# Performance work log

Measured on AMD Instinct MI355X. Metric: run time of the kernel, lower is better.

Reference implementation:

```python
import jax, jax.numpy as jnp
import numpy as np

D_MODEL = 1024
NUM_HEADS = 16
KERNEL_EPS = 1e-4
NORM_STAB = 1e-6


def setup_inputs() -> dict:
    key = jax.random.key(0)
    k1, k2, k3, k4 = jax.random.split(key, 4)
    B, L = 4, 2048
    d_head, m = D_MODEL // NUM_HEADS, 256
    return {
        "query": jax.random.normal(k1, (B, L, D_MODEL), jnp.float32),
        "key": jax.random.normal(k2, (B, L, D_MODEL), jnp.float32),
        "value": jax.random.normal(k3, (B, L, D_MODEL), jnp.float32),
        # random projection matrix (fixed, not learned); original uses orthogonal blocks
        "random_features": jax.random.normal(k4, (d_head, m), jnp.float32),
    }


def _performer_forward(query, key, value, random_features):
    B, L, dm = query.shape
    h = NUM_HEADS
    d = dm // h
    m = random_features.shape[1]

    def split_heads(x):  # [B,L,dm] -> [B,h,L,d]
        return x.reshape(B, L, h, d).transpose(0, 2, 1, 3)

    q, k, v = split_heads(query), split_heads(key), split_heads(value)

    # FAVOR+ exp kernel with stabilizers (matches get_projected_queries_and_keys)
    scale = dm ** -0.25
    q = q * scale
    k = k * scale
    proj_q = jnp.einsum('bhld,dm->bhlm', q, random_features)
    proj_k = jnp.einsum('bhld,dm->bhlm', k, random_features)
    h_q = -0.5 * jnp.sum(q * q, axis=-1, keepdims=True)  # [B,h,L,1]
    h_k = -0.5 * jnp.sum(k * k, axis=-1, keepdims=True)
    q_stab = h_q  # reduce_max over a keepdims size-1 axis == identity (faithful)
    k_stab = jnp.max(h_k)  # global scalar
    q_kernel = jnp.exp(h_q + (proj_q - q_stab))
    k_kernel = jnp.exp(h_k + (proj_k - k_stab))
    nc = m ** -0.5
    q_prime = nc * (q_kernel + KERNEL_EPS)  # [B,h,L,m]
    k_prime = nc * (k_kernel + KERNEL_EPS)

    # Causal linear attention: streaming prefix state instead of [B,h,L,m,d] cumsum
    qp = q_prime.transpose(2, 0, 1, 3)  # [L,B,h,m]
    kp = k_prime.transpose(2, 0, 1, 3)
    vp = v.transpose(2, 0, 1, 3)        # [L,B,h,d]

    def step(carry, inp):
        S, Z = carry                      # S:[B,h,m,d], Z:[B,h,m]
        qt, kt, vt = inp
        S = S + kt[..., :, None] * vt[..., None, :]
        Z = Z + kt
        num = jnp.einsum('bhm,bhmd->bhd', qt, S)
        den = jnp.einsum('bhm,bhm->bh', qt, Z)
        return (S, Z), (num, den)

    S0 = jnp.zeros((B, h, m, d), q_prime.dtype)
    Z0 = jnp.zeros((B, h, m), q_prime.dtype)
    _, (nums, dens) = jax.lax.scan(step, (S0, Z0), (qp, kp, vp))
    nums = nums.transpose(1, 2, 0, 3)          # [B,h,L,d]
    dens = dens.transpose(1, 2, 0)[..., None]  # [B,h,L,1]

    # stabilize denominator near zero (matches _denominator_...)
    extreme = (jnp.abs(dens) <= NORM_STAB).astype(dens.dtype)
    dens = dens + 2.0 * NORM_STAB * extreme
    out = nums / dens

    # merge heads -> [B,L,dm]
    return out.transpose(0, 2, 1, 3).reshape(B, L, dm)


def reference(query, key, value, random_features):
    return _performer_forward(query, key, value, random_features)
```

## Files before the change

### kernel.cpp

```cpp
#include <hip/hip_runtime.h>


#define BB 4
#define HH 16
#define LL 2048
#define DH 64
#define DM 1024
#define MM 256
#define CC 64
#define NCH (LL / CC)

constexpr float SCALE = 0.17677669529663687f;
constexpr float NCF   = 0.0625f;
constexpr float LNCF  = -2.772588722239781f;
constexpr float KEPS  = 1e-4f;
constexpr float NCFK  = NCF * KEPS;
constexpr float NSTB  = 1e-6f;

typedef __attribute__((ext_vector_type(8))) short s16x8;
typedef __attribute__((ext_vector_type(4))) float f32x4;

__device__ __forceinline__ float bf2f(unsigned short s) {
  return __uint_as_float(((unsigned)s) << 16);
}
__device__ __forceinline__ unsigned short f2bf(float f) {
  return __builtin_bit_cast(unsigned short, static_cast<__bf16>(f));
}
__device__ __forceinline__ unsigned enc_key(float f) {
  unsigned u = __float_as_uint(f);
  return (u & 0x80000000u) ? ~u : (u | 0x80000000u);
}
__device__ __forceinline__ float dec_key(unsigned k) {
  unsigned u = (k & 0x80000000u) ? (k & 0x7FFFFFFFu) : ~k;
  return __uint_as_float(u);
}

__global__ __launch_bounds__(256) void kstab_kernel(const float* __restrict__ Kin,
                                                    unsigned int* __restrict__ wsu) {
  int lane = threadIdx.x & 63;
  int wave = threadIdx.x >> 6;
  int base = blockIdx.x * 64 + wave * 16;
  float m = -3.4e38f;
  for (int it = 0; it < 16; ++it) {
    int r = base + it;
    float v = Kin[(size_t)r * 64 + lane];
    float s = v * v;
    #pragma unroll
    for (int off = 32; off; off >>= 1) s += __shfl_xor(s, off, 64);
    float hk = -0.5f * (SCALE * SCALE) * s;
    m = fmaxf(m, hk);
  }
  __shared__ float wmax[4];
  if (lane == 0) wmax[wave] = m;
  __syncthreads();
  if (threadIdx.x == 0) {
    float mm = fmaxf(fmaxf(wmax[0], wmax[1]), fmaxf(wmax[2], wmax[3]));
    atomicMax(wsu, enc_key(mm));
  }
}

__global__ __launch_bounds__(256) void rft_prep(const float* __restrict__ RF,
                                                unsigned short* __restrict__ RFTg) {
  int m = threadIdx.x;
  float rv[64];
  #pragma unroll
  for (int d = 0; d < 64; ++d) rv[d] = RF[d * MM + m];
  unsigned swz = (unsigned)((m & 7) << 4);
  #pragma unroll
  for (int c16 = 0; c16 < 8; ++c16) {
    union { unsigned short u[8]; uint4 v; } pk_;
    #pragma unroll
    for (int i = 0; i < 8; ++i) pk_.u[i] = f2bf(rv[c16 * 8 + i]);
    unsigned byte = (unsigned)(m * 128) + (((unsigned)(c16 * 16)) ^ swz);
    *(uint4*)((char*)RFTg + byte) = pk_.v;
  }
}

__global__ __launch_bounds__(256) void phase1_kernel(const float* __restrict__ Kin,
                                                     const float* __restrict__ Vin,
                                                     const unsigned short* __restrict__ RFTg,
                                                     unsigned short* __restrict__ wsSb,
                                                     float* __restrict__ wsZ,
                                                     const unsigned int* __restrict__ wsu,
                                                     int bh0) {
  __shared__ __align__(16) char lds[45056];
  char* U0  = lds;
  char* KPl = lds + 16384;
  char* VT  = lds + 32768;
  float* Zw = (float*)(lds + 40960);

  int slice = blockIdx.x / NCH;
  int c     = blockIdx.x % NCH;
  int bh = bh0 + slice, b = bh >> 4, h = bh & 15;
  const int t    = threadIdx.x;
  const int lane = t & 63;
  const int w    = t >> 6;
  const int rloc = lane & 15;
  const int kc0  = (lane >> 4) * 8;
  const int arow = 16 * w + rloc;
  const unsigned lgrp16 = (unsigned)((lane >> 4) * 16);
  float kst = dec_key(*wsu);

  const float* krow = Kin + ((size_t)(b * LL + c * CC + arow)) * DM + h * DH;
  s16x8 kfrag[2];
  float ss = 0.f;
  #pragma unroll
  for (int kf = 0; kf < 2; ++kf) {
    float4 ka_ = *(const float4*)(krow + kf * 32 + kc0);
    float4 kb_ = *(const float4*)(krow + kf * 32 + kc0 + 4);
    float ks[8] = {ka_.x, ka_.y, ka_.z, ka_.w, kb_.x, kb_.y, kb_.z, kb_.w};
    #pragma unroll
    for (int i = 0; i < 8; ++i) {
      float kv = ks[i] * SCALE;
      ss += kv * kv;
      kfrag[kf][i] = (short)f2bf(kv);
    }
  }
  ss += __shfl_xor(ss, 16, 64);
  ss += __shfl_xor(ss, 32, 64);
  float hkv = -0.5f * ss;
  float hkb[4];
  #pragma unroll
  for (int r = 0; r < 4; ++r)
    hkb[r] = __shfl(hkv, (lane >> 4) * 4 + r, 64) - kst + LNCF;

  {
    const float* vbase = Vin + ((size_t)(b * LL + c * CC + w * 16)) * DM + h * DH + lane;
    float vv[16];
    #pragma unroll
    for (int i = 0; i < 16; ++i) vv[i] = vbase[(size_t)i * DM];
    unsigned swz = (unsigned)((lane & 7) << 4);
    #pragma unroll
    for (int q = 0; q < 2; ++q) {
      union { unsigned short u[8]; uint4 v; } pk_;
      #pragma unroll
      for (int i = 0; i < 8; ++i) pk_.u[i] = f2bf(vv[q * 8 + i]);
      unsigned byte = (unsigned)(lane * 128) + (((unsigned)(w * 32 + q * 16)) ^ swz);
      *(uint4*)(VT + byte) = pk_.v;
    }
  }

  for (int h2 = 0; h2 < 2; ++h2) {
    __syncthreads();
    {
      const uint4* src = (const uint4*)(RFTg + (size_t)h2 * 8192);
      uint4* dst = (uint4*)U0;
      #pragma unroll
      for (int r2 = 0; r2 < 4; ++r2) dst[t + 256 * r2] = src[t + 256 * r2];
    }
    __syncthreads();

    f32x4 pk[8];
    #pragma unroll
    for (int i = 0; i < 8; ++i) pk[i] = (f32x4)0.f;
    #pragma unroll
    for (int mt = 0; mt < 8; ++mt) {
      int mloc = mt * 16 + rloc;
      unsigned rbyte = (unsigned)(mloc * 128);
      unsigned swz = (unsigned)((mloc & 7) << 4);
      #pragma unroll
      for (int kf = 0; kf < 2; ++kf) {
        s16x8 bf_ = *(const s16x8*)(U0 + rbyte + (((unsigned)(kf * 64) + lgrp16) ^ swz));
        pk[mt] = __builtin_amdgcn_mfma_f32_16x16x32_bf16(kfrag[kf], bf_, pk[mt], 0, 0, 0);
      }
    }
    #pragma unroll
    for (int mt = 0; mt < 8; ++mt) {
      int mloc = mt * 16 + rloc;
      float zp = 0.f;
      #pragma unroll
      for (int r = 0; r < 4; ++r) {
        int cpos = 16 * w + (lane >> 4) * 4 + r;
        float kpv = __expf(hkb[r] + pk[mt][r]) + NCFK;
        zp += kpv;
        unsigned byte = (unsigned)(mloc * 128) +
                        (((unsigned)(cpos * 2)) ^ ((unsigned)((mloc & 7) << 4)));
        *(unsigned short*)(KPl + byte) = f2bf(kpv);
      }
      zp += __shfl_xor(zp, 16, 64);
      zp += __shfl_xor(zp, 32, 64);
      if (lane < 16) Zw[w * 256 + h2 * 128 + mt * 16 + lane] = zp;
    }
    __syncthreads();

    f32x4 sacc[8];
    #pragma unroll
    for (int i = 0; i < 8; ++i) sacc[i] = (f32x4)0.f;
    s16x8 af[2];
    {
      int drow = w * 16 + rloc;
      unsigned rbyte = (unsigned)(drow * 128);
      unsigned swz = (unsigned)((drow & 7) << 4);
      #pragma unroll
      for (int kf = 0; kf < 2; ++kf)
        af[kf] = *(const s16x8*)(VT + rbyte + (((unsigned)(kf * 64) + lgrp16) ^ swz));
    }
    #pragma unroll
    for (int mt = 0; mt < 8; ++mt) {
      int mrow = mt * 16 + rloc;
      unsigned rbyte = (unsigned)(mrow * 128);
      unsigned swz = (unsigned)((mrow & 7) << 4);
      #pragma unroll
      for (int kf = 0; kf < 2; ++kf) {
        s16x8 bf_ = *(const s16x8*)(KPl + rbyte + (((unsigned)(kf * 64) + lgrp16) ^ swz));
        sacc[mt] = __builtin_amdgcn_mfma_f32_16x16x32_bf16(af[kf], bf_, sacc[mt], 0, 0, 0);
      }
    }
    unsigned short* sdst = wsSb + (size_t)(slice * NCH + c) * 16384;
    #pragma unroll
    for (int mt = 0; mt < 8; ++mt) {
      #pragma unroll
      for (int r = 0; r < 4; ++r) {
        int d = w * 16 + (lane >> 4) * 4 + r;
        int m = h2 * 128 + mt * 16 + rloc;
        sdst[d * 256 + m] = f2bf(sacc[mt][r]);
      }
    }
  }
  __syncthreads();
  float z = Zw[t] + Zw[256 + t] + Zw[512 + t] + Zw[768 + t];
  wsZ[(size_t)(slice * NCH + c) * MM + t] = z;
}

__global__ __launch_bounds__(256) void scan_kernel(const unsigned short* __restrict__ wsSb,
                                                   unsigned short* __restrict__ wsPb,
                                                   float* __restrict__ wsZ) {
  int slice = blockIdx.x >> 3, part = blockIdx.x & 7;
  const int t = threadIdx.x;
  int d_l = t >> 5, moct = t & 31;
  int d = part * 8 + d_l, m0 = moct * 8;
  int half = m0 >> 7, m_l = m0 & 127;
  const unsigned short* srcb = wsSb + (size_t)slice * NCH * 16384 + d * 256 + m0;
  char* dstb = (char*)wsPb + ((size_t)slice * NCH * 2 + half) * 16384 +
               (unsigned)(d * 256) + (((unsigned)(m_l * 2)) ^ ((unsigned)((d & 7) << 4)));
  float run[8] = {0.f, 0.f, 0.f, 0.f, 0.f, 0.f, 0.f, 0.f};
  for (int c = 0; c < NCH; ++c) {
    uint4 v = *(const uint4*)(srcb + (size_t)c * 16384);
    union { unsigned short u[8]; uint4 q; } o;
    #pragma unroll
    for (int i = 0; i < 8; ++i) o.u[i] = f2bf(run[i]);
    *(uint4*)(dstb + (size_t)c * 32768) = o.q;
    const unsigned short* pv = (const unsigned short*)&v;
    #pragma unroll
    for (int i = 0; i < 8; ++i) run[i] += bf2f(pv[i]);
  }
  if (part == 0) {
    for (int e = t; e < MM; e += 256) {
      float zr = 0.f;
      for (int c = 0; c < NCH; ++c) {
        size_t idx = (size_t)slice * NCH * MM + (size_t)c * MM + e;
        float x = wsZ[idx];
        wsZ[idx] = zr;
        zr += x;
      }
    }
  }
}

__global__ __launch_bounds__(256) void phase3_kernel(const float* __restrict__ Qin,
                                                     const float* __restrict__ Kin,
                                                     const float* __restrict__ Vin,
                                                     const unsigned short* __restrict__ RFTg,
                                                     const unsigned short* __restrict__ wsPb,
                                                     const float* __restrict__ wsZ,
                                                     const unsigned int* __restrict__ wsu,
                                                     float* __restrict__ Out,
                                                     int bh0) {
  __shared__ __align__(16) char lds[50176];
  char* U0  = lds;
  char* QPl = lds + 16384;
  char* KPl = lds + 32768;
  float* ZL = (float*)(lds + 49152);

  int slice = blockIdx.x / NCH;
  int c     = blockIdx.x % NCH;
  int bh = bh0 + slice, b = bh >> 4, h = bh & 15;
  const int t    = threadIdx.x;
  const int lane = t & 63;
  const int w    = t >> 6;

  ZL[t] = wsZ[(size_t)(slice * NCH + c) * MM + t];
  float kst = dec_key(*wsu);

  const int rloc = lane & 15;
  const int kc0  = (lane >> 4) * 8;
  const int arow = 16 * w + rloc;
  const float* qrow = Qin + ((size_t)(b * LL + c * CC + arow)) * DM + h * DH;
  const float* krow = Kin + ((size_t)(b * LL + c * CC + arow)) * DM + h * DH;

  s16x8 qfrag[2], kfrag[2];
  float ss = 0.f;
  #pragma unroll
  for (int kf = 0; kf < 2; ++kf) {
    float4 qa_ = *(const float4*)(qrow + kf * 32 + kc0);
    float4 qb_ = *(const float4*)(qrow + kf * 32 + kc0 + 4);
    float4 ka_ = *(const float4*)(krow + kf * 32 + kc0);
    float4 kb_ = *(const float4*)(krow + kf * 32 + kc0 + 4);
    float qs[8] = {qa_.x, qa_.y, qa_.z, qa_.w, qb_.x, qb_.y, qb_.z, qb_.w};
    float ks[8] = {ka_.x, ka_.y, ka_.z, ka_.w, kb_.x, kb_.y, kb_.z, kb_.w};
    #pragma unroll
    for (int i = 0; i < 8; ++i) {
      float qv = qs[i] * SCALE, kv = ks[i] * SCALE;
      ss += kv * kv;
      qfrag[kf][i] = (short)f2bf(qv);
      kfrag[kf][i] = (short)f2bf(kv);
    }
  }
  ss += __shfl_xor(ss, 16, 64);
  ss += __shfl_xor(ss, 32, 64);
  float hkv = -0.5f * ss;

  f32x4 Aacc[4], Oacc[4];
  #pragma unroll
  for (int i = 0; i < 4; ++i) { Aacc[i] = (f32x4)0.f; Oacc[i] = (f32x4)0.f; }
  float den1[4] = {0.f, 0.f, 0.f, 0.f};
  float den2[4] = {0.f, 0.f, 0.f, 0.f};

  float hkb[4];
  #pragma unroll
  for (int r = 0; r < 4; ++r)
    hkb[r] = __shfl(hkv, (lane >> 4) * 4 + r, 64) - kst + LNCF;

  const unsigned lgrp16 = (unsigned)((lane >> 4) * 16);

  for (int h2 = 0; h2 < 2; ++h2) {
    __syncthreads();
    {
      const uint4* src = (const uint4*)(RFTg + (size_t)h2 * 8192);
      uint4* dst = (uint4*)U0;
      #pragma unroll
      for (int r2 = 0; r2 < 4; ++r2) dst[t + 256 * r2] = src[t + 256 * r2];
    }
    __syncthreads();

    f32x4 pq[8], pk[8];
    #pragma unroll
    for (int i = 0; i < 8; ++i) { pq[i] = (f32x4)0.f; pk[i] = (f32x4)0.f; }
    #pragma unroll
    for (int mt = 0; mt < 8; ++mt) {
      int mloc = mt * 16 + rloc;
      unsigned rbyte = (unsigned)(mloc * 128);
      unsigned swz = (unsigned)((mloc & 7) << 4);
      #pragma unroll
      for (int kf = 0; kf < 2; ++kf) {
        s16x8 bf_ = *(const s16x8*)(U0 + rbyte + (((unsigned)(kf * 64) + lgrp16) ^ swz));
        pq[mt] = __builtin_amdgcn_mfma_f32_16x16x32_bf16(qfrag[kf], bf_, pq[mt], 0, 0, 0);
        pk[mt] = __builtin_amdgcn_mfma_f32_16x16x32_bf16(kfrag[kf], bf_, pk[mt], 0, 0, 0);
      }
    }
    #pragma unroll
    for (int mt = 0; mt < 8; ++mt) {
      int mloc = mt * 16 + rloc;
      #pragma unroll
      for (int r = 0; r < 4; ++r) {
        int row = 16 * w + (lane >> 4) * 4 + r;
        float qpv = __expf(pq[mt][r] + LNCF) + NCFK;
        float kpv = __expf(hkb[r] + pk[mt][r]) + NCFK;
        unsigned byte = (unsigned)(row * 256) +
                        (((unsigned)(mloc * 2)) ^ ((unsigned)((row & 7) << 4)));
        *(unsigned short*)(QPl + byte) = f2bf(qpv);
        *(unsigned short*)(KPl + byte) = f2bf(kpv);
        den2[r] += qpv * ZL[h2 * 128 + mloc];
      }
    }
    __syncthreads();

    uint4 stmp[4];
    {
      const char* ssrc = (const char*)wsPb + ((size_t)(slice * NCH + c) * 2 + h2) * 16384;
      #pragma unroll
      for (int r2 = 0; r2 < 4; ++r2)
        stmp[r2] = *(const uint4*)(ssrc + t * 16 + r2 * 4096);
    }

    s16x8 qa[4];
    {
      unsigned rbyte = (unsigned)(arow * 256);
      unsigned swz = (unsigned)((arow & 7) << 4);
      #pragma unroll
      for (int kf = 0; kf < 4; ++kf)
        qa[kf] = *(const s16x8*)(QPl + rbyte + (((unsigned)(kf * 64) + lgrp16) ^ swz));
    }
    for (int ct = 0; ct <= w; ++ct) {
      int rowb = ct * 16 + rloc;
      unsigned rbyte = (unsigned)(rowb * 256);
      unsigned swz = (unsigned)((rowb & 7) << 4);
      #pragma unroll
      for (int kf = 0; kf < 4; ++kf) {
        s16x8 bf_ = *(const s16x8*)(KPl + rbyte + (((unsigned)(kf * 64) + lgrp16) ^ swz));
        Aacc[ct] = __builtin_amdgcn_mfma_f32_16x16x32_bf16(qa[kf], bf_, Aacc[ct], 0, 0, 0);
      }
    }
    {
      uint4* u0v = (uint4*)U0;
      #pragma unroll
      for (int r2 = 0; r2 < 4; ++r2) u0v[t + 256 * r2] = stmp[r2];
    }
    __syncthreads();

    #pragma unroll
    for (int ct = 0; ct < 4; ++ct) {
      int rowb = ct * 16 + rloc;
      unsigned rbyte = (unsigned)(rowb * 256);
      unsigned swz = (unsigned)((rowb & 7) << 4);
      #pragma unroll
      for (int kf = 0; kf < 4; ++kf) {
        s16x8 bf_ = *(const s16x8*)(U0 + rbyte + (((unsigned)(kf * 64) + lgrp16) ^ swz));
        Oacc[ct] = __builtin_amdgcn_mfma_f32_16x16x32_bf16(qa[kf], bf_, Oacc[ct], 0, 0, 0);
      }
    }
  }

  __syncthreads();

  #pragma unroll
  for (int ct = 0; ct < 4; ++ct) {
    #pragma unroll
    for (int r = 0; r < 4; ++r) {
      int row = 16 * w + (lane >> 4) * 4 + r;
      int col = ct * 16 + rloc;
      float av = (ct <= w && col <= row) ? Aacc[ct][r] : 0.f;
      den1[r] += av;
      unsigned byte = (unsigned)(row * 128) +
                      (((unsigned)(col * 2)) ^ ((unsigned)((row & 7) << 4)));
      *(unsigned short*)(U0 + byte) = f2bf(av);
    }
  }
  {
    const float* vbase = Vin + ((size_t)(b * LL + c * CC + w * 16)) * DM + h * DH + lane;
    float vv[16];
    #pragma unroll
    for (int i = 0; i < 16; ++i) vv[i] = vbase[(size_t)i * DM];
    unsigned swz = (unsigned)((lane & 7) << 4);
    #pragma unroll
    for (int q = 0; q < 2; ++q) {
      union { unsigned short u[8]; uint4 v; } pk_;
      #pragma unroll
      for (int i = 0; i < 8; ++i) pk_.u[i] = f2bf(vv[q * 8 + i]);
      unsigned byte = 8192u + (unsigned)(lane * 128) + (((unsigned)(w * 32 + q * 16)) ^ swz);
      *(uint4*)(U0 + byte) = pk_.v;
    }
  }
  __syncthreads();

  {
    int nkf = (w >= 2) ? 2 : 1;
    unsigned arbyte = (unsigned)(arow * 128);
    unsigned aswz = (unsigned)((arow & 7) << 4);
    for (int kf = 0; kf < nkf; ++kf) {
      s16x8 af = *(const s16x8*)(U0 + arbyte + (((unsigned)(kf * 64) + lgrp16) ^ aswz));
      #pragma unroll
      for (int ct = 0; ct < 4; ++ct) {
        int rowv = ct * 16 + rloc;
        unsigned byte = 8192u + (unsigned)(rowv * 128) +
                        (((unsigned)(kf * 64) + lgrp16) ^ ((unsigned)((rowv & 7) << 4)));
        s16x8 vf = *(const s16x8*)(U0 + byte);
        Oacc[ct] = __builtin_amdgcn_mfma_f32_16x16x32_bf16(af, vf, Oacc[ct], 0, 0, 0);
      }
    }
  }

  float inv[4];
  #pragma unroll
  for (int r = 0; r < 4; ++r) {
    float dv = den1[r] + den2[r];
    dv += __shfl_xor(dv, 1, 64);
    dv += __shfl_xor(dv, 2, 64);
    dv += __shfl_xor(dv, 4, 64);
    dv += __shfl_xor(dv, 8, 64);
    if (fabsf(dv) <= NSTB) dv += 2.f * NSTB;
    inv[r] = 1.0f / dv;
  }
  #pragma unroll
  for (int r = 0; r < 4; ++r) {
    int row = 16 * w + (lane >> 4) * 4 + r;
    size_t g = ((size_t)(b * LL + c * CC + row)) * DM + h * DH;
    #pragma unroll
    for (int ct = 0; ct < 4; ++ct) {
      Out[g + ct * 16 + rloc] = Oacc[ct][r] * inv[r];
    }
  }
}

extern "C" void kernel_launch(void* const* d_in, const int* in_sizes, int n_in,
                              void* d_out, int out_size, void* d_ws, size_t ws_size,
                              hipStream_t stream) {
  const float* Q  = (const float*)d_in[0];
  const float* K  = (const float*)d_in[1];
  const float* V  = (const float*)d_in[2];
  const float* RF = (const float*)d_in[3];
  float* Out = (float*)d_out;
  unsigned int* wsu = (unsigned int*)d_ws;

  const size_t RESV = 1024;
  const size_t RFTB = 32768;
  const size_t perSlice = (size_t)NCH * 16384 * 2
                        + (size_t)NCH * 2 * 16384
                        + (size_t)NCH * MM * 4;
  int G = BB * HH;
  while (G > 1 && RESV + RFTB + (size_t)G * perSlice > ws_size) G >>= 1;

  unsigned short* RFTg = (unsigned short*)((char*)d_ws + RESV);
  unsigned short* wsSb = (unsigned short*)((char*)d_ws + RESV + RFTB);
  unsigned short* wsPb = wsSb + (size_t)G * NCH * 16384;
  float* wsZ = (float*)((char*)wsPb + (size_t)G * NCH * 2 * 16384);

  hipMemsetAsync(d_ws, 0, 4, stream);
  hipLaunchKernelGGL(kstab_kernel, dim3(2048), dim3(256), 0, stream, K, wsu);
  hipLaunchKernelGGL(rft_prep, dim3(1), dim3(256), 0, stream, RF, RFTg);
  for (int bh0 = 0; bh0 < BB * HH; bh0 += G) {
    hipLaunchKernelGGL(phase1_kernel, dim3(G * NCH), dim3(256), 0, stream,
                       K, V, RFTg, wsSb, wsZ, wsu, bh0);
    hipLaunchKernelGGL(scan_kernel, dim3(G * 8), dim3(256), 0, stream, wsSb, wsPb, wsZ);
    hipLaunchKernelGGL(phase3_kernel, dim3(G * NCH), dim3(256), 0, stream,
                       Q, K, V, RFTg, wsPb, wsZ, wsu, Out, bh0);
  }
}
```

Baseline: 160.9 us.

## Repartition phase1 projection by m-columns per wave and overwrite RF buffer in place

Each wave now loads all 64 key rows of the chunk as MFMA fragments and computes the projection for its own 32 random-feature columns, instead of 16 rows against all 128 columns. The exp'd kernel values are written back into the same LDS rows that held the random features, which removes the separate K' buffer and the four-way Z partial reduction. This cuts the LDS footprint from about 44KB to 25KB, which may allow more resident blocks. The cost is four times the key fragment registers per thread and some extra shuffles for the row norms.

```diff
diff --git a/kernel.cpp b/kernel.cpp
--- a/kernel.cpp
+++ b/kernel.cpp
@@ -83,11 +83,10 @@
                                                      float* __restrict__ wsZ,
                                                      const unsigned int* __restrict__ wsu,
                                                      int bh0) {
-  __shared__ __align__(16) char lds[45056];
-  char* U0  = lds;
-  char* KPl = lds + 16384;
-  char* VT  = lds + 32768;
-  float* Zw = (float*)(lds + 40960);
+  __shared__ __align__(16) char lds[25600];
+  char* B0  = lds;
+  char* VT  = lds + 16384;
+  float* Zw = (float*)(lds + 24576);
 
   int slice = blockIdx.x / NCH;
   int c     = blockIdx.x % NCH;
@@ -97,32 +96,31 @@
   const int w    = t >> 6;
   const int rloc = lane & 15;
   const int kc0  = (lane >> 4) * 8;
-  const int arow = 16 * w + rloc;
   const unsigned lgrp16 = (unsigned)((lane >> 4) * 16);
   float kst = dec_key(*wsu);
 
-  const float* krow = Kin + ((size_t)(b * LL + c * CC + arow)) * DM + h * DH;
-  s16x8 kfrag[2];
-  float ss = 0.f;
-  #pragma unroll
-  for (int kf = 0; kf < 2; ++kf) {
-    float4 ka_ = *(const float4*)(krow + kf * 32 + kc0);
-    float4 kb_ = *(const float4*)(krow + kf * 32 + kc0 + 4);
-    float ks[8] = {ka_.x, ka_.y, ka_.z, ka_.w, kb_.x, kb_.y, kb_.z, kb_.w};
-    #pragma unroll
-    for (int i = 0; i < 8; ++i) {
-      float kv = ks[i] * SCALE;
-      ss += kv * kv;
-      kfrag[kf][i] = (short)f2bf(kv);
-    }
-  }
-  ss += __shfl_xor(ss, 16, 64);
-  ss += __shfl_xor(ss, 32, 64);
-  float hkv = -0.5f * ss;
-  float hkb[4];
-  #pragma unroll
-  for (int r = 0; r < 4; ++r)
-    hkb[r] = __shfl(hkv, (lane >> 4) * 4 + r, 64) - kst + LNCF;
+  s16x8 kfrag[4][2];
+  float hkv[4];
+  #pragma unroll
+  for (int rb = 0; rb < 4; ++rb) {
+    const float* krow = Kin + ((size_t)(b * LL + c * CC + rb * 16 + rloc)) * DM + h * DH;
+    float ss = 0.f;
+    #pragma unroll
+    for (int kf = 0; kf < 2; ++kf) {
+      float4 ka_ = *(const float4*)(krow + kf * 32 + kc0);
+      float4 kb_ = *(const float4*)(krow + kf * 32 + kc0 + 4);
+      float ks[8] = {ka_.x, ka_.y, ka_.z, ka_.w, kb_.x, kb_.y, kb_.z, kb_.w};
+      #pragma unroll
+      for (int i = 0; i < 8; ++i) {
+        float kv = ks[i] * SCALE;
+        ss += kv * kv;
+        kfrag[rb][kf][i] = (short)f2bf(kv);
+      }
+    }
+    ss += __shfl_xor(ss, 16, 64);
+    ss += __shfl_xor(ss, 32, 64);
+    hkv[rb] = -0.5f * ss - kst + LNCF;
+  }
 
   {
     const float* vbase = Vin + ((size_t)(b * LL + c * CC + w * 16)) * DM + h * DH + lane;
@@ -144,42 +142,44 @@
     __syncthreads();
     {
       const uint4* src = (const uint4*)(RFTg + (size_t)h2 * 8192);
-      uint4* dst = (uint4*)U0;
+      uint4* dst = (uint4*)B0;
       #pragma unroll
       for (int r2 = 0; r2 < 4; ++r2) dst[t + 256 * r2] = src[t + 256 * r2];
     }
     __syncthreads();
 
-    f32x4 pk[8];
-    #pragma unroll
-    for (int i = 0; i < 8; ++i) pk[i] = (f32x4)0.f;
-    #pragma unroll
-    for (int mt = 0; mt < 8; ++mt) {
-      int mloc = mt * 16 + rloc;
+    #pragma unroll
+    for (int mq = 0; mq < 2; ++mq) {
+      int mloc = w * 32 + mq * 16 + rloc;
       unsigned rbyte = (unsigned)(mloc * 128);
       unsigned swz = (unsigned)((mloc & 7) << 4);
-      #pragma unroll
-      for (int kf = 0; kf < 2; ++kf) {
-        s16x8 bf_ = *(const s16x8*)(U0 + rbyte + (((unsigned)(kf * 64) + lgrp16) ^ swz));
-        pk[mt] = __builtin_amdgcn_mfma_f32_16x16x32_bf16(kfrag[kf], bf_, pk[mt], 0, 0, 0);
-      }
-    }
-    #pragma unroll
-    for (int mt = 0; mt < 8; ++mt) {
-      int mloc = mt * 16 + rloc;
+      s16x8 bfr[2];
+      #pragma unroll
+      for (int kf = 0; kf < 2; ++kf)
+        bfr[kf] = *(const s16x8*)(B0 + rbyte + (((unsigned)(kf * 64) + lgrp16) ^ swz));
+      f32x4 pk[4];
+      #pragma unroll
+      for (int rb = 0; rb < 4; ++rb) pk[rb] = (f32x4)0.f;
+      #pragma unroll
+      for (int rb = 0; rb < 4; ++rb)
+        #pragma unroll
+        for (int kf = 0; kf < 2; ++kf)
+          pk[rb] = __builtin_amdgcn_mfma_f32_16x16x32_bf16(kfrag[rb][kf], bfr[kf], pk[rb], 0, 0, 0);
       float zp = 0.f;
       #pragma unroll
-      for (int r = 0; r < 4; ++r) {
-        int cpos = 16 * w + (lane >> 4) * 4 + r;
-        float kpv = __expf(hkb[r] + pk[mt][r]) + NCFK;
-        zp += kpv;
-        unsigned byte = (unsigned)(mloc * 128) +
-                        (((unsigned)(cpos * 2)) ^ ((unsigned)((mloc & 7) << 4)));
-        *(unsigned short*)(KPl + byte) = f2bf(kpv);
+      for (int rb = 0; rb < 4; ++rb) {
+        #pragma unroll
+        for (int r = 0; r < 4; ++r) {
+          float hkr = __shfl(hkv[rb], (lane >> 4) * 4 + r, 64);
+          float kpv = __expf(hkr + pk[rb][r]) + NCFK;
+          zp += kpv;
+          int cpos = rb * 16 + (lane >> 4) * 4 + r;
+          *(unsigned short*)(B0 + rbyte + (((unsigned)(cpos * 2)) ^ swz)) = f2bf(kpv);
+        }
       }
       zp += __shfl_xor(zp, 16, 64);
       zp += __shfl_xor(zp, 32, 64);
-      if (lane < 16) Zw[w * 256 + h2 * 128 + mt * 16 + lane] = zp;
+      if (lane < 16) Zw[h2 * 128 + w * 32 + mq * 16 + lane] = zp;
     }
     __syncthreads();
 
@@ -202,7 +202,7 @@
       unsigned swz = (unsigned)((mrow & 7) << 4);
       #pragma unroll
       for (int kf = 0; kf < 2; ++kf) {
-        s16x8 bf_ = *(const s16x8*)(KPl + rbyte + (((unsigned)(kf * 64) + lgrp16) ^ swz));
+        s16x8 bf_ = *(const s16x8*)(B0 + rbyte + (((unsigned)(kf * 64) + lgrp16) ^ swz));
         sacc[mt] = __builtin_amdgcn_mfma_f32_16x16x32_bf16(af[kf], bf_, sacc[mt], 0, 0, 0);
       }
     }
@@ -218,8 +218,7 @@
     }
   }
   __syncthreads();
-  float z = Zw[t] + Zw[256 + t] + Zw[512 + t] + Zw[768 + t];
-  wsZ[(size_t)(slice * NCH + c) * MM + t] = z;
+  wsZ[(size_t)(slice * NCH + c) * MM + t] = Zw[t];
 }
 
 __global__ __launch_bounds__(256) void scan_kernel(const unsigned short* __restrict__ wsSb,
```

Result: no change. 162.9 us (+1.2%).
